# Kernel optimization log

Measured on AMD Instinct MI355X. Metric: run time of the kernel, lower is better.

The kernel has to match this reference:

```python
import jax, jax.numpy as jnp
import numpy as np

WINDOW_SIZE = 128

def setup_inputs() -> dict:
    key = jax.random.key(0)
    kq, kk, kv = jax.random.split(key, 3)
    B, S, D = 4, 4096, 128
    q = jax.random.normal(kq, (B, S, D), dtype=jnp.float32)
    k = jax.random.normal(kk, (B, S, D), dtype=jnp.float32)
    v = jax.random.normal(kv, (B, S, D), dtype=jnp.float32)
    return {"q": q, "k": k, "v": v}

def reference(q, k, v):
    B, S, D = q.shape
    q = q / jnp.sqrt(jnp.asarray(D, q.dtype))
    # band mask: tril(window_size-1) & triu(-(window_size-1)) == |i - j| <= window_size-1
    i = jax.lax.broadcasted_iota(jnp.int32, (S, S), 0)
    j = jax.lax.broadcasted_iota(jnp.int32, (S, S), 1)
    mask = jnp.abs(i - j) <= (WINDOW_SIZE - 1)
    scores = jnp.einsum('bqd,bkd->bqk', q, k)  # [B,S,S]
    scores = jnp.where(mask, scores, jnp.asarray(-1e9, scores.dtype))
    weights = jax.nn.softmax(scores, axis=-1)
    return jnp.einsum('bqk,bkd->bqd', weights, v)
```

## Files before the change

kernel.cpp:

```cpp
#include <hip/hip_runtime.h>


typedef __attribute__((ext_vector_type(8))) _Float16 half8;
typedef __attribute__((ext_vector_type(2))) __fp16 fp16x2;
typedef __attribute__((ext_vector_type(4))) float floatx4;

#define MFMA_F16(a, b, c) __builtin_amdgcn_mfma_f32_16x16x32_f16(a, b, c, 0, 0, 0)

constexpr int S_ = 4096, D_ = 128, W_ = 127;
constexpr int BQ = 64, BK = 64;
constexpr int PST = 72;
constexpr int OST = 132;

union SMem {
  struct {
    _Float16 Kh[2][BK * D_];
    _Float16 Vt[2][D_ * BK];
    _Float16 Ps[4][16 * PST];
  } a;
  struct {
    float Om[8][16 * OST];
    float l_[8][16];
  } b;
};

__device__ __forceinline__ unsigned pk2(float a, float b) {
  union { fp16x2 h; unsigned u; } c;
  c.h = __builtin_amdgcn_cvt_pkrtz(a, b);
  return c.u;
}

__device__ __forceinline__ void gll16(const _Float16* g, _Float16* l) {
  __builtin_amdgcn_global_load_lds(
      (const __attribute__((address_space(1))) void*)g,
      (__attribute__((address_space(3))) void*)l, 16, 0, 0);
}

__global__ __launch_bounds__(256, 4)
void prep_kernel(const float* __restrict__ kg, const float* __restrict__ vg,
                 _Float16* __restrict__ K16, _Float16* __restrict__ Vt16)
{
  __shared__ __align__(16) _Float16 Vs[BK * D_];
  const int t  = threadIdx.x;
  const int bb = blockIdx.x >> 6;
  const int c  = blockIdx.x & 63;
  const size_t base = ((size_t)bb * S_ + c * 64) * D_;

#pragma unroll
  for (int j = 0; j < 4; ++j) {
    const int id = t + 256 * j;
    const int s = id >> 4, blk = id & 15;
    const float* src = kg + base + s * D_ + blk * 8;
    float4 a  = *(const float4*)src;
    float4 b2 = *(const float4*)(src + 4);
    uint4 w;
    w.x = pk2(a.x, a.y);  w.y = pk2(a.z, a.w);
    w.z = pk2(b2.x, b2.y); w.w = pk2(b2.z, b2.w);
    *(uint4*)(K16 + base + s * D_ + 8 * (blk ^ (s & 7))) = w;
  }

  const int vr = t >> 5, vc = t & 31;
  float4 vf[8];
#pragma unroll
  for (int u = 0; u < 8; ++u)
    vf[u] = *(const float4*)(vg + base + (8 * vr + u) * D_ + 4 * vc);
#pragma unroll
  for (int i = 0; i < 4; ++i) {
    uint4 tv;
    tv.x = pk2(((const float*)&vf[0])[i], ((const float*)&vf[1])[i]);
    tv.y = pk2(((const float*)&vf[2])[i], ((const float*)&vf[3])[i]);
    tv.z = pk2(((const float*)&vf[4])[i], ((const float*)&vf[5])[i]);
    tv.w = pk2(((const float*)&vf[6])[i], ((const float*)&vf[7])[i]);
    const int d = 4 * vc + i;
    *(uint4*)(&Vs[d * 64 + 8 * (vr ^ (d & 7))]) = tv;
  }
  __syncthreads();
  _Float16* vdst = Vt16 + (size_t)(bb * 64 + c) * (D_ * 64);
#pragma unroll
  for (int i = 0; i < 4; ++i) {
    const int id2 = t + 256 * i;
    *(uint4*)(vdst + id2 * 8) = *(const uint4*)(&Vs[id2 * 8]);
  }
}

__global__ __launch_bounds__(512, 2)
void swa_v6_kernel(const float* __restrict__ qg,
                   const _Float16* __restrict__ K16,
                   const _Float16* __restrict__ Vt16,
                   float* __restrict__ og)
{
  __shared__ __align__(16) SMem sm;
  const int tid  = threadIdx.x;
  const int lane = tid & 63;
  const int wave = tid >> 6;
  const int lx   = lane & 15;
  const int quad = lane >> 4;
  const int tile = wave & 3;
  const int par  = wave >> 2;

  const int bid = blockIdx.x;
  const int lid = (bid & 7) * 32 + (bid >> 3);
  const int bb  = lid >> 6;
  const int q0  = (lid & 63) * BQ;

  const float* qb = qg + (size_t)bb * S_ * D_;
  float*       ob = og + (size_t)bb * S_ * D_;

  const int qrow = q0 + 16 * tile + lx;
  half8 qh[4], ql[4];
#pragma unroll
  for (int ks = 0; ks < 4; ++ks) {
    const float* p = qb + (size_t)qrow * D_ + 32 * ks + 8 * quad;
#pragma unroll
    for (int j = 0; j < 8; ++j) {
      float f = p[j];
      _Float16 h = (_Float16)f;
      qh[ks][j] = h;
      ql[ks][j] = (_Float16)(f - (float)h);
    }
  }

  floatx4 o[8];
#pragma unroll
  for (int dt = 0; dt < 8; ++dt) o[dt] = (floatx4){0.f, 0.f, 0.f, 0.f};
  float lp[4] = {0.f, 0.f, 0.f, 0.f};

  const int kstart = (q0 > W_) ? (q0 - W_) : 0;
  int kend = q0 + BQ - 1 + W_;
  if (kend > S_ - 1) kend = S_ - 1;
  const int c0 = kstart >> 6, c1 = kend >> 6;

  const int ilo = q0 + 16 * tile, ihi = ilo + 15;
  const float C1 = 0.12751727f, C2 = -5.7707802f;

  const int wk = (wave < 4) ? wave : (wave - 4);

  {
    const int b0 = c0 & 1;
    const _Float16* kcb = K16 + ((size_t)bb * S_ + c0 * 64) * D_;
    const _Float16* vcb = Vt16 + (size_t)(bb * 64 + c0) * (D_ * 64);
#pragma unroll
    for (int i = 0; i < 4; ++i) {
      const int ofs = (wk * 4 + i) * 512;
      if (wave < 4) gll16(kcb + ofs + lane * 8, &sm.a.Kh[b0][ofs]);
      else          gll16(vcb + ofs + lane * 8, &sm.a.Vt[b0][ofs]);
    }
  }

  for (int c = c0; c <= c1; ++c) {
    const int buf = c & 1;
    asm volatile("s_waitcnt vmcnt(0)" ::: "memory");
    __builtin_amdgcn_s_barrier();
    asm volatile("" ::: "memory");

    if (c < c1) {
      const _Float16* kcb = K16 + ((size_t)bb * S_ + (c + 1) * 64) * D_;
      const _Float16* vcb = Vt16 + (size_t)(bb * 64 + (c + 1)) * (D_ * 64);
#pragma unroll
      for (int i = 0; i < 4; ++i) {
        const int ofs = (wk * 4 + i) * 512;
        if (wave < 4) gll16(kcb + ofs + lane * 8, &sm.a.Kh[buf ^ 1][ofs]);
        else          gll16(vcb + ofs + lane * 8, &sm.a.Vt[buf ^ 1][ofs]);
      }
    }

    if (((c - c0) & 1) != par) continue;
    const int kc = c * BK;
    if (kc + BK - 1 < ilo - W_ || kc > ihi + W_) continue;

    floatx4 acc[4];
#pragma unroll
    for (int ct = 0; ct < 4; ++ct) acc[ct] = (floatx4){0.f, 0.f, 0.f, 0.f};
#pragma unroll
    for (int ks = 0; ks < 4; ++ks) {
#pragma unroll
      for (int ct = 0; ct < 4; ++ct) {
        const int row = 16 * ct + lx;
        half8 bfr = *(const half8*)(
            &sm.a.Kh[buf][row * D_ + 8 * ((4 * ks + quad) ^ (lx & 7))]);
        acc[ct] = MFMA_F16(qh[ks], bfr, acc[ct]);
        acc[ct] = MFMA_F16(ql[ks], bfr, acc[ct]);
      }
    }

    const int ibase = q0 + 16 * tile + 4 * quad;
#pragma unroll
    for (int r = 0; r < 4; ++r) {
      const int i = ibase + r;
      float psum = 0.f;
#pragma unroll
      for (int ct = 0; ct < 4; ++ct) {
        const int col = kc + 16 * ct + lx;
        const bool v = (unsigned)(col - i + W_) <= (unsigned)(2 * W_);
        const float e = __builtin_amdgcn_exp2f(__builtin_fmaf(acc[ct][r], C1, C2));
        const float p = v ? e : 0.f;
        psum += p;
        sm.a.Ps[tile][(4 * quad + r) * PST + 16 * ct + lx] = (_Float16)p;
      }
      lp[r] += psum;
    }
    asm volatile("s_waitcnt lgkmcnt(0)" ::: "memory");
    half8 pa0 = *(const half8*)(&sm.a.Ps[tile][lx * PST + 8 * quad]);
    half8 pa1 = *(const half8*)(&sm.a.Ps[tile][lx * PST + 32 + 8 * quad]);

#pragma unroll
    for (int dt = 0; dt < 8; ++dt) {
      const int d = 16 * dt + lx;
      half8 v0 = *(const half8*)(&sm.a.Vt[buf][d * 64 + 8 * (quad ^ (d & 7))]);
      half8 v1 = *(const half8*)(&sm.a.Vt[buf][d * 64 + 8 * ((4 + quad) ^ (d & 7))]);
      o[dt] = MFMA_F16(pa0, v0, o[dt]);
      o[dt] = MFMA_F16(pa1, v1, o[dt]);
    }
  }

#pragma unroll
  for (int r = 0; r < 4; ++r) {
    float s = lp[r];
    s += __shfl_xor(s, 1);
    s += __shfl_xor(s, 2);
    s += __shfl_xor(s, 4);
    s += __shfl_xor(s, 8);
    lp[r] = s;
  }

  __syncthreads();
#pragma unroll
  for (int dt = 0; dt < 8; ++dt)
#pragma unroll
    for (int r = 0; r < 4; ++r)
      sm.b.Om[wave][(4 * quad + r) * OST + 16 * dt + lx] = o[dt][r];
  if (lx == 0) {
#pragma unroll
    for (int r = 0; r < 4; ++r) sm.b.l_[wave][4 * quad + r] = lp[r];
  }
  __syncthreads();

  const int row = tid >> 3, cd = tid & 7;
  const int tl = row >> 4, r16 = row & 15;
  const float inv = 1.f / (sm.b.l_[tl][r16] + sm.b.l_[tl + 4][r16]);
  const float* Oa = &sm.b.Om[tl][r16 * OST + 16 * cd];
  const float* Ob = &sm.b.Om[tl + 4][r16 * OST + 16 * cd];
  float* dst = ob + (size_t)(q0 + row) * D_ + 16 * cd;
#pragma unroll
  for (int t = 0; t < 4; ++t) {
    float4 xa = *(const float4*)(Oa + 4 * t);
    float4 xb = *(const float4*)(Ob + 4 * t);
    float4 r4;
    r4.x = (xa.x + xb.x) * inv;
    r4.y = (xa.y + xb.y) * inv;
    r4.z = (xa.z + xb.z) * inv;
    r4.w = (xa.w + xb.w) * inv;
    *(float4*)(dst + 4 * t) = r4;
  }
}

extern "C" void kernel_launch(void* const* d_in, const int* in_sizes, int n_in,
                              void* d_out, int out_size, void* d_ws, size_t ws_size,
                              hipStream_t stream) {
  const float* q = (const float*)d_in[0];
  const float* k = (const float*)d_in[1];
  const float* v = (const float*)d_in[2];
  float* out = (float*)d_out;

  const int B = in_sizes[0] / (S_ * D_);
  _Float16* K16  = (_Float16*)d_ws;
  _Float16* Vt16 = (_Float16*)d_ws + (size_t)B * S_ * D_;

  prep_kernel<<<dim3(B * (S_ / BK)), dim3(256), 0, stream>>>(k, v, K16, Vt16);
  swa_v6_kernel<<<dim3(B * (S_ / BQ)), dim3(512), 0, stream>>>(q, K16, Vt16, out);
}
```

Before: 88.59 us.

## Drop key-chunk parity split; use 4 waves per block processing all chunks

The block shrinks from 8 waves to 4. Each wave now handles every key chunk for its 16-row query tile, where before two wave groups split the chunks by parity and merged their partial outputs through shared memory. This removes the cross-wave reduction buffer and the final summation, and normalises in registers before a plain copy-out. The cost is less parallelism per block: each wave now does twice the MFMA work serially, and each wave issues twice as many K/V loads.

Result: no change. 89.44 us (+1.0%).

```diff
diff --git a/kernel.cpp b/kernel.cpp
--- a/kernel.cpp
+++ b/kernel.cpp
@@ -19,8 +19,7 @@
     _Float16 Ps[4][16 * PST];
   } a;
   struct {
-    float Om[8][16 * OST];
-    float l_[8][16];
+    float Om[4][16 * OST];
   } b;
 };
 
@@ -83,8 +82,8 @@
   }
 }
 
-__global__ __launch_bounds__(512, 2)
-void swa_v6_kernel(const float* __restrict__ qg,
+__global__ __launch_bounds__(256, 2)
+void swa_v7_kernel(const float* __restrict__ qg,
                    const _Float16* __restrict__ K16,
                    const _Float16* __restrict__ Vt16,
                    float* __restrict__ og)
@@ -95,8 +94,6 @@
   const int wave = tid >> 6;
   const int lx   = lane & 15;
   const int quad = lane >> 4;
-  const int tile = wave & 3;
-  const int par  = wave >> 2;
 
   const int bid = blockIdx.x;
   const int lid = (bid & 7) * 32 + (bid >> 3);
@@ -106,7 +103,7 @@
   const float* qb = qg + (size_t)bb * S_ * D_;
   float*       ob = og + (size_t)bb * S_ * D_;
 
-  const int qrow = q0 + 16 * tile + lx;
+  const int qrow = q0 + 16 * wave + lx;
   half8 qh[4], ql[4];
 #pragma unroll
   for (int ks = 0; ks < 4; ++ks) {
@@ -130,20 +127,21 @@
   if (kend > S_ - 1) kend = S_ - 1;
   const int c0 = kstart >> 6, c1 = kend >> 6;
 
-  const int ilo = q0 + 16 * tile, ihi = ilo + 15;
+  const int ilo = q0 + 16 * wave, ihi = ilo + 15;
   const float C1 = 0.12751727f, C2 = -5.7707802f;
 
-  const int wk = (wave < 4) ? wave : (wave - 4);
+  const int sh  = wave >> 1;
+  const int sub = wave & 1;
 
   {
     const int b0 = c0 & 1;
     const _Float16* kcb = K16 + ((size_t)bb * S_ + c0 * 64) * D_;
     const _Float16* vcb = Vt16 + (size_t)(bb * 64 + c0) * (D_ * 64);
 #pragma unroll
-    for (int i = 0; i < 4; ++i) {
-      const int ofs = (wk * 4 + i) * 512;
-      if (wave < 4) gll16(kcb + ofs + lane * 8, &sm.a.Kh[b0][ofs]);
-      else          gll16(vcb + ofs + lane * 8, &sm.a.Vt[b0][ofs]);
+    for (int i = 0; i < 8; ++i) {
+      const int ofs = (sub * 8 + i) * 512;
+      if (sh == 0) gll16(kcb + ofs + lane * 8, &sm.a.Kh[b0][ofs]);
+      else         gll16(vcb + ofs + lane * 8, &sm.a.Vt[b0][ofs]);
     }
   }
 
@@ -157,14 +155,13 @@
       const _Float16* kcb = K16 + ((size_t)bb * S_ + (c + 1) * 64) * D_;
       const _Float16* vcb = Vt16 + (size_t)(bb * 64 + (c + 1)) * (D_ * 64);
 #pragma unroll
-      for (int i = 0; i < 4; ++i) {
-        const int ofs = (wk * 4 + i) * 512;
-        if (wave < 4) gll16(kcb + ofs + lane * 8, &sm.a.Kh[buf ^ 1][ofs]);
-        else          gll16(vcb + ofs + lane * 8, &sm.a.Vt[buf ^ 1][ofs]);
+      for (int i = 0; i < 8; ++i) {
+        const int ofs = (sub * 8 + i) * 512;
+        if (sh == 0) gll16(kcb + ofs + lane * 8, &sm.a.Kh[buf ^ 1][ofs]);
+        else         gll16(vcb + ofs + lane * 8, &sm.a.Vt[buf ^ 1][ofs]);
       }
     }
 
-    if (((c - c0) & 1) != par) continue;
     const int kc = c * BK;
     if (kc + BK - 1 < ilo - W_ || kc > ihi + W_) continue;
 
@@ -183,7 +180,7 @@
       }
     }
 
-    const int ibase = q0 + 16 * tile + 4 * quad;
+    const int ibase = q0 + 16 * wave + 4 * quad;
 #pragma unroll
     for (int r = 0; r < 4; ++r) {
       const int i = ibase + r;
@@ -195,13 +192,13 @@
         const float e = __builtin_amdgcn_exp2f(__builtin_fmaf(acc[ct][r], C1, C2));
         const float p = v ? e : 0.f;
         psum += p;
-        sm.a.Ps[tile][(4 * quad + r) * PST + 16 * ct + lx] = (_Float16)p;
+        sm.a.Ps[wave][(4 * quad + r) * PST + 16 * ct + lx] = (_Float16)p;
       }
       lp[r] += psum;
     }
     asm volatile("s_waitcnt lgkmcnt(0)" ::: "memory");
-    half8 pa0 = *(const half8*)(&sm.a.Ps[tile][lx * PST + 8 * quad]);
-    half8 pa1 = *(const half8*)(&sm.a.Ps[tile][lx * PST + 32 + 8 * quad]);
+    half8 pa0 = *(const half8*)(&sm.a.Ps[wave][lx * PST + 8 * quad]);
+    half8 pa1 = *(const half8*)(&sm.a.Ps[wave][lx * PST + 32 + 8 * quad]);
 
 #pragma unroll
     for (int dt = 0; dt < 8; ++dt) {
@@ -213,6 +210,7 @@
     }
   }
 
+  float inv[4];
 #pragma unroll
   for (int r = 0; r < 4; ++r) {
     float s = lp[r];
@@ -220,7 +218,7 @@
     s += __shfl_xor(s, 2);
     s += __shfl_xor(s, 4);
     s += __shfl_xor(s, 8);
-    lp[r] = s;
+    inv[r] = 1.f / s;
   }
 
   __syncthreads();
@@ -228,30 +226,16 @@
   for (int dt = 0; dt < 8; ++dt)
 #pragma unroll
     for (int r = 0; r < 4; ++r)
-      sm.b.Om[wave][(4 * quad + r) * OST + 16 * dt + lx] = o[dt][r];
-  if (lx == 0) {
-#pragma unroll
-    for (int r = 0; r < 4; ++r) sm.b.l_[wave][4 * quad + r] = lp[r];
-  }
+      sm.b.Om[wave][(4 * quad + r) * OST + 16 * dt + lx] = o[dt][r] * inv[r];
   __syncthreads();
 
-  const int row = tid >> 3, cd = tid & 7;
+  const int row = tid >> 2, seg = tid & 3;
   const int tl = row >> 4, r16 = row & 15;
-  const float inv = 1.f / (sm.b.l_[tl][r16] + sm.b.l_[tl + 4][r16]);
-  const float* Oa = &sm.b.Om[tl][r16 * OST + 16 * cd];
-  const float* Ob = &sm.b.Om[tl + 4][r16 * OST + 16 * cd];
-  float* dst = ob + (size_t)(q0 + row) * D_ + 16 * cd;
-#pragma unroll
-  for (int t = 0; t < 4; ++t) {
-    float4 xa = *(const float4*)(Oa + 4 * t);
-    float4 xb = *(const float4*)(Ob + 4 * t);
-    float4 r4;
-    r4.x = (xa.x + xb.x) * inv;
-    r4.y = (xa.y + xb.y) * inv;
-    r4.z = (xa.z + xb.z) * inv;
-    r4.w = (xa.w + xb.w) * inv;
-    *(float4*)(dst + 4 * t) = r4;
-  }
+  const float* src = &sm.b.Om[tl][r16 * OST + 32 * seg];
+  float* dst = ob + (size_t)(q0 + row) * D_ + 32 * seg;
+#pragma unroll
+  for (int t = 0; t < 8; ++t)
+    *(float4*)(dst + 4 * t) = *(const float4*)(src + 4 * t);
 }
 
 extern "C" void kernel_launch(void* const* d_in, const int* in_sizes, int n_in,
@@ -267,5 +251,5 @@
   _Float16* Vt16 = (_Float16*)d_ws + (size_t)B * S_ * D_;
 
   prep_kernel<<<dim3(B * (S_ / BK)), dim3(256), 0, stream>>>(k, v, K16, Vt16);
-  swa_v6_kernel<<<dim3(B * (S_ / BQ)), dim3(512), 0, stream>>>(q, K16, Vt16, out);
-}
+  swa_v7_kernel<<<dim3(B * (S_ / BQ)), dim3(256), 0, stream>>>(q, K16, Vt16, out);
+}
```

## Load K/V fragments directly from global into registers, drop LDS staging

Applied to the files above, without the earlier changes.

The attention kernel no longer stages K and V chunks through double-buffered LDS with barriers. Each wave now loads its MFMA fragments straight from global memory (relying on L2 for reuse) into registers, and the prep kernel writes unswizzled layouts to match. The block shrinks to 32 query rows and 4 waves, so the grid doubles. Each 16-row tile also gets its own key range, which trims chunk iterations at the edges. This removes barrier sync and LDS traffic but adds redundant global loads across waves, plus register pressure from holding 32 fragment vectors.

Measured after the change: 98.71 us. 1.11x slower.

```diff
diff --git a/kernel.cpp b/kernel.cpp
--- a/kernel.cpp
+++ b/kernel.cpp
@@ -8,21 +8,8 @@
 #define MFMA_F16(a, b, c) __builtin_amdgcn_mfma_f32_16x16x32_f16(a, b, c, 0, 0, 0)
 
 constexpr int S_ = 4096, D_ = 128, W_ = 127;
-constexpr int BQ = 64, BK = 64;
 constexpr int PST = 72;
 constexpr int OST = 132;
-
-union SMem {
-  struct {
-    _Float16 Kh[2][BK * D_];
-    _Float16 Vt[2][D_ * BK];
-    _Float16 Ps[4][16 * PST];
-  } a;
-  struct {
-    float Om[8][16 * OST];
-    float l_[8][16];
-  } b;
-};
 
 __device__ __forceinline__ unsigned pk2(float a, float b) {
   union { fp16x2 h; unsigned u; } c;
@@ -30,17 +17,11 @@
   return c.u;
 }
 
-__device__ __forceinline__ void gll16(const _Float16* g, _Float16* l) {
-  __builtin_amdgcn_global_load_lds(
-      (const __attribute__((address_space(1))) void*)g,
-      (__attribute__((address_space(3))) void*)l, 16, 0, 0);
-}
-
 __global__ __launch_bounds__(256, 4)
 void prep_kernel(const float* __restrict__ kg, const float* __restrict__ vg,
                  _Float16* __restrict__ K16, _Float16* __restrict__ Vt16)
 {
-  __shared__ __align__(16) _Float16 Vs[BK * D_];
+  __shared__ __align__(16) _Float16 Vs[64 * D_];
   const int t  = threadIdx.x;
   const int bb = blockIdx.x >> 6;
   const int c  = blockIdx.x & 63;
@@ -56,7 +37,7 @@
     uint4 w;
     w.x = pk2(a.x, a.y);  w.y = pk2(a.z, a.w);
     w.z = pk2(b2.x, b2.y); w.w = pk2(b2.z, b2.w);
-    *(uint4*)(K16 + base + s * D_ + 8 * (blk ^ (s & 7))) = w;
+    *(uint4*)(K16 + base + s * D_ + 8 * blk) = w;
   }
 
   const int vr = t >> 5, vc = t & 31;
@@ -79,32 +60,38 @@
 #pragma unroll
   for (int i = 0; i < 4; ++i) {
     const int id2 = t + 256 * i;
-    *(uint4*)(vdst + id2 * 8) = *(const uint4*)(&Vs[id2 * 8]);
-  }
-}
-
-__global__ __launch_bounds__(512, 2)
-void swa_v6_kernel(const float* __restrict__ qg,
+    const int d = id2 >> 3, g = id2 & 7;
+    *(uint4*)(vdst + id2 * 8) = *(const uint4*)(&Vs[d * 64 + 8 * (g ^ (d & 7))]);
+  }
+}
+
+__global__ __launch_bounds__(256, 2)
+void swa_v8_kernel(const float* __restrict__ qg,
                    const _Float16* __restrict__ K16,
                    const _Float16* __restrict__ Vt16,
                    float* __restrict__ og)
 {
-  __shared__ __align__(16) SMem sm;
+  __shared__ __align__(16) _Float16 Ps[4][16 * PST];
+  __shared__ __align__(16) float    Om[4][16 * OST];
+  __shared__ float Ls[4][16];
+
   const int tid  = threadIdx.x;
   const int lane = tid & 63;
   const int wave = tid >> 6;
   const int lx   = lane & 15;
   const int quad = lane >> 4;
-  const int tile = wave & 3;
-  const int par  = wave >> 2;
+  const int tile = wave & 1;
+  const int kh   = wave >> 1;
 
   const int bid = blockIdx.x;
-  const int lid = (bid & 7) * 32 + (bid >> 3);
-  const int bb  = lid >> 6;
-  const int q0  = (lid & 63) * BQ;
+  const int lid = (bid & 7) * 64 + (bid >> 3);
+  const int bb  = lid >> 7;
+  const int q0  = (lid & 127) * 32;
 
   const float* qb = qg + (size_t)bb * S_ * D_;
   float*       ob = og + (size_t)bb * S_ * D_;
+  const _Float16* Kb = K16 + (size_t)bb * S_ * D_;
+  const _Float16* Vb = Vt16 + (size_t)bb * 64 * (D_ * 64);
 
   const int qrow = q0 + 16 * tile + lx;
   half8 qh[4], ql[4];
@@ -125,64 +112,43 @@
   for (int dt = 0; dt < 8; ++dt) o[dt] = (floatx4){0.f, 0.f, 0.f, 0.f};
   float lp[4] = {0.f, 0.f, 0.f, 0.f};
 
-  const int kstart = (q0 > W_) ? (q0 - W_) : 0;
-  int kend = q0 + BQ - 1 + W_;
+  const int ilo = q0 + 16 * tile, ihi = ilo + 15;
+  const int kstart = (ilo > W_) ? (ilo - W_) : 0;
+  int kend = ihi + W_;
   if (kend > S_ - 1) kend = S_ - 1;
   const int c0 = kstart >> 6, c1 = kend >> 6;
 
-  const int ilo = q0 + 16 * tile, ihi = ilo + 15;
   const float C1 = 0.12751727f, C2 = -5.7707802f;
 
-  const int wk = (wave < 4) ? wave : (wave - 4);
-
-  {
-    const int b0 = c0 & 1;
-    const _Float16* kcb = K16 + ((size_t)bb * S_ + c0 * 64) * D_;
-    const _Float16* vcb = Vt16 + (size_t)(bb * 64 + c0) * (D_ * 64);
-#pragma unroll
-    for (int i = 0; i < 4; ++i) {
-      const int ofs = (wk * 4 + i) * 512;
-      if (wave < 4) gll16(kcb + ofs + lane * 8, &sm.a.Kh[b0][ofs]);
-      else          gll16(vcb + ofs + lane * 8, &sm.a.Vt[b0][ofs]);
-    }
-  }
-
-  for (int c = c0; c <= c1; ++c) {
-    const int buf = c & 1;
-    asm volatile("s_waitcnt vmcnt(0)" ::: "memory");
-    __builtin_amdgcn_s_barrier();
-    asm volatile("" ::: "memory");
-
-    if (c < c1) {
-      const _Float16* kcb = K16 + ((size_t)bb * S_ + (c + 1) * 64) * D_;
-      const _Float16* vcb = Vt16 + (size_t)(bb * 64 + (c + 1)) * (D_ * 64);
-#pragma unroll
-      for (int i = 0; i < 4; ++i) {
-        const int ofs = (wk * 4 + i) * 512;
-        if (wave < 4) gll16(kcb + ofs + lane * 8, &sm.a.Kh[buf ^ 1][ofs]);
-        else          gll16(vcb + ofs + lane * 8, &sm.a.Vt[buf ^ 1][ofs]);
+  for (int c = c0 + kh; c <= c1; c += 2) {
+    const _Float16* kc_ = Kb + (size_t)c * 64 * D_;
+    const _Float16* vc_ = Vb + (size_t)c * (D_ * 64);
+
+    half8 kfr[4][4];
+#pragma unroll
+    for (int ks = 0; ks < 4; ++ks)
+#pragma unroll
+      for (int ct = 0; ct < 4; ++ct)
+        kfr[ks][ct] = *(const half8*)(kc_ + (16 * ct + lx) * D_ + 32 * ks + 8 * quad);
+    half8 vfr[8][2];
+#pragma unroll
+    for (int dt = 0; dt < 8; ++dt)
+#pragma unroll
+      for (int h2 = 0; h2 < 2; ++h2)
+        vfr[dt][h2] = *(const half8*)(vc_ + (16 * dt + lx) * 64 + 32 * h2 + 8 * quad);
+
+    floatx4 acc[4];
+#pragma unroll
+    for (int ct = 0; ct < 4; ++ct) acc[ct] = (floatx4){0.f, 0.f, 0.f, 0.f};
+#pragma unroll
+    for (int ks = 0; ks < 4; ++ks)
+#pragma unroll
+      for (int ct = 0; ct < 4; ++ct) {
+        acc[ct] = MFMA_F16(qh[ks], kfr[ks][ct], acc[ct]);
+        acc[ct] = MFMA_F16(ql[ks], kfr[ks][ct], acc[ct]);
       }
-    }
-
-    if (((c - c0) & 1) != par) continue;
-    const int kc = c * BK;
-    if (kc + BK - 1 < ilo - W_ || kc > ihi + W_) continue;
-
-    floatx4 acc[4];
-#pragma unroll
-    for (int ct = 0; ct < 4; ++ct) acc[ct] = (floatx4){0.f, 0.f, 0.f, 0.f};
-#pragma unroll
-    for (int ks = 0; ks < 4; ++ks) {
-#pragma unroll
-      for (int ct = 0; ct < 4; ++ct) {
-        const int row = 16 * ct + lx;
-        half8 bfr = *(const half8*)(
-            &sm.a.Kh[buf][row * D_ + 8 * ((4 * ks + quad) ^ (lx & 7))]);
-        acc[ct] = MFMA_F16(qh[ks], bfr, acc[ct]);
-        acc[ct] = MFMA_F16(ql[ks], bfr, acc[ct]);
-      }
-    }
-
+
+    const int kc = c * 64;
     const int ibase = q0 + 16 * tile + 4 * quad;
 #pragma unroll
     for (int r = 0; r < 4; ++r) {
@@ -195,21 +161,18 @@
         const float e = __builtin_amdgcn_exp2f(__builtin_fmaf(acc[ct][r], C1, C2));
         const float p = v ? e : 0.f;
         psum += p;
-        sm.a.Ps[tile][(4 * quad + r) * PST + 16 * ct + lx] = (_Float16)p;
+        Ps[wave][(4 * quad + r) * PST + 16 * ct + lx] = (_Float16)p;
       }
       lp[r] += psum;
     }
     asm volatile("s_waitcnt lgkmcnt(0)" ::: "memory");
-    half8 pa0 = *(const half8*)(&sm.a.Ps[tile][lx * PST + 8 * quad]);
-    half8 pa1 = *(const half8*)(&sm.a.Ps[tile][lx * PST + 32 + 8 * quad]);
+    half8 pa0 = *(const half8*)(&Ps[wave][lx * PST + 8 * quad]);
+    half8 pa1 = *(const half8*)(&Ps[wave][lx * PST + 32 + 8 * quad]);
 
 #pragma unroll
     for (int dt = 0; dt < 8; ++dt) {
-      const int d = 16 * dt + lx;
-      half8 v0 = *(const half8*)(&sm.a.Vt[buf][d * 64 + 8 * (quad ^ (d & 7))]);
-      half8 v1 = *(const half8*)(&sm.a.Vt[buf][d * 64 + 8 * ((4 + quad) ^ (d & 7))]);
-      o[dt] = MFMA_F16(pa0, v0, o[dt]);
-      o[dt] = MFMA_F16(pa1, v1, o[dt]);
+      o[dt] = MFMA_F16(pa0, vfr[dt][0], o[dt]);
+      o[dt] = MFMA_F16(pa1, vfr[dt][1], o[dt]);
     }
   }
 
@@ -223,23 +186,22 @@
     lp[r] = s;
   }
 
-  __syncthreads();
 #pragma unroll
   for (int dt = 0; dt < 8; ++dt)
 #pragma unroll
     for (int r = 0; r < 4; ++r)
-      sm.b.Om[wave][(4 * quad + r) * OST + 16 * dt + lx] = o[dt][r];
+      Om[wave][(4 * quad + r) * OST + 16 * dt + lx] = o[dt][r];
   if (lx == 0) {
 #pragma unroll
-    for (int r = 0; r < 4; ++r) sm.b.l_[wave][4 * quad + r] = lp[r];
+    for (int r = 0; r < 4; ++r) Ls[wave][4 * quad + r] = lp[r];
   }
   __syncthreads();
 
   const int row = tid >> 3, cd = tid & 7;
   const int tl = row >> 4, r16 = row & 15;
-  const float inv = 1.f / (sm.b.l_[tl][r16] + sm.b.l_[tl + 4][r16]);
-  const float* Oa = &sm.b.Om[tl][r16 * OST + 16 * cd];
-  const float* Ob = &sm.b.Om[tl + 4][r16 * OST + 16 * cd];
+  const float inv = 1.f / (Ls[tl][r16] + Ls[tl + 2][r16]);
+  const float* Oa = &Om[tl][r16 * OST + 16 * cd];
+  const float* Ob = &Om[tl + 2][r16 * OST + 16 * cd];
   float* dst = ob + (size_t)(q0 + row) * D_ + 16 * cd;
 #pragma unroll
   for (int t = 0; t < 4; ++t) {
@@ -266,6 +228,6 @@
   _Float16* K16  = (_Float16*)d_ws;
   _Float16* Vt16 = (_Float16*)d_ws + (size_t)B * S_ * D_;
 
-  prep_kernel<<<dim3(B * (S_ / BK)), dim3(256), 0, stream>>>(k, v, K16, Vt16);
-  swa_v6_kernel<<<dim3(B * (S_ / BQ)), dim3(512), 0, stream>>>(q, K16, Vt16, out);
-}
+  prep_kernel<<<dim3(B * 64), dim3(256), 0, stream>>>(k, v, K16, Vt16);
+  swa_v8_kernel<<<dim3(B * 128), dim3(256), 0, stream>>>(q, K16, Vt16, out);
+}
```
